# Performance work log

Measured on AMD Instinct MI355X. Metric: run time of the kernel, lower is better.

The kernel has to match this reference:

```python
import jax, jax.numpy as jnp
import numpy as np

N_NODES = 100000
N_EDGES = 1600000
NODE_DIM = 5
HIDDEN = 64
N_LAYERS = 3


def setup_inputs() -> dict:
    key = jax.random.key(0)
    ks = jax.random.split(key, 12)
    s = 0.1
    return {
        "x": jax.random.normal(ks[0], (N_NODES, NODE_DIM), dtype=jnp.float32),
        "edge_index": jax.random.randint(ks[1], (2, N_EDGES), 0, N_NODES, dtype=jnp.int32),
        # message MLP params per layer (stacked over layers)
        "W1": jax.random.normal(ks[2], (N_LAYERS, 2 * NODE_DIM, HIDDEN), dtype=jnp.float32) * s,
        "b1": jnp.zeros((N_LAYERS, HIDDEN), dtype=jnp.float32),
        "W2": jax.random.normal(ks[3], (N_LAYERS, HIDDEN, NODE_DIM), dtype=jnp.float32) * s,
        "b2": jnp.zeros((N_LAYERS, NODE_DIM), dtype=jnp.float32),
        # update MLP params per layer
        "U1": jax.random.normal(ks[4], (N_LAYERS, 2 * NODE_DIM, HIDDEN), dtype=jnp.float32) * s,
        "bu1": jnp.zeros((N_LAYERS, HIDDEN), dtype=jnp.float32),
        "U2": jax.random.normal(ks[5], (N_LAYERS, HIDDEN, NODE_DIM), dtype=jnp.float32) * s,
        "bu2": jnp.zeros((N_LAYERS, NODE_DIM), dtype=jnp.float32),
        # readout
        "Wr": jax.random.normal(ks[6], (NODE_DIM, NODE_DIM), dtype=jnp.float32) * s,
        "br": jnp.zeros((NODE_DIM,), dtype=jnp.float32),
    }


def reference(x, edge_index, W1, b1, W2, b2, U1, bu1, U2, bu2, Wr, br):
    # PyG convention: messages flow from source j = edge_index[0] to target i = edge_index[1]
    src = edge_index[0]
    dst = edge_index[1]
    n = x.shape[0]
    for l in range(N_LAYERS):
        x_i = x[dst]                                   # [E, d] target features
        x_j = x[src]                                   # [E, d] source features
        msg_in = jnp.concatenate([x_i, x_j], axis=-1)  # [E, 2d]
        msg = jax.nn.relu(msg_in @ W1[l] + b1[l]) @ W2[l] + b2[l]   # [E, d]
        aggr = jax.ops.segment_sum(msg, dst, num_segments=n)        # [N, d] scatter-add at targets
        upd_in = jnp.concatenate([x, aggr], axis=-1)   # [N, 2d]
        upd = jax.nn.relu(upd_in @ U1[l] + bu1[l]) @ U2[l] + bu2[l]  # [N, d]
        x = upd + x                                    # residual (in SkeletonGNN.forward)
    return x @ Wr + br
```

## Files before the change

kernel.cpp:

```cpp
#include <hip/hip_runtime.h>

#define N_NODES 100000
#define N_EDGES 1600000
#define DIM 5
#define HID 64
#define N_LAYERS 3
#define SCAN_BLK 256
#define NBLK ((N_NODES + SCAN_BLK - 1) / SCAN_BLK)

__global__ __launch_bounds__(256) void fused_hist_msg1_kernel(
    const float* __restrict__ x,
    const int* __restrict__ ei,
    const float* __restrict__ W1, const float* __restrict__ b1,
    const float* __restrict__ W2, const float* __restrict__ b2,
    int* __restrict__ cnt, int* __restrict__ rank,
    float* __restrict__ msg0)
{
    int e = blockIdx.x * blockDim.x + threadIdx.x;
    if (e >= N_EDGES) return;
    int src = ei[e];
    int dst = ei[N_EDGES + e];

    int rk = atomicAdd(&cnt[dst], 1);

    float in[10];
    const float* xi = x + (long)dst * DIM;
    const float* xj = x + (long)src * DIM;
#pragma unroll
    for (int d = 0; d < DIM; ++d) in[d] = xi[d];
#pragma unroll
    for (int d = 0; d < DIM; ++d) in[DIM + d] = xj[d];

    float msg[DIM];
#pragma unroll
    for (int j = 0; j < DIM; ++j) msg[j] = b2[j];

#pragma unroll 8
    for (int h = 0; h < HID; ++h) {
        float acc = b1[h];
#pragma unroll
        for (int d = 0; d < 10; ++d) acc = fmaf(in[d], W1[d * HID + h], acc);
        acc = fmaxf(acc, 0.0f);
#pragma unroll
        for (int j = 0; j < DIM; ++j) msg[j] = fmaf(acc, W2[h * DIM + j], msg[j]);
    }

    float* mp = msg0 + (long)e * DIM;
#pragma unroll
    for (int j = 0; j < DIM; ++j) mp[j] = msg[j];

    rank[e] = rk;
}


__global__ __launch_bounds__(SCAN_BLK) void scan_part_kernel(
    const int* __restrict__ cnt, int* __restrict__ blk_sum)
{
    __shared__ int s[SCAN_BLK];
    int t = threadIdx.x;
    int i = blockIdx.x * SCAN_BLK + t;
    s[t] = (i < N_NODES) ? cnt[i] : 0;
    __syncthreads();
    for (int off = SCAN_BLK / 2; off > 0; off >>= 1) {
        if (t < off) s[t] += s[t + off];
        __syncthreads();
    }
    if (t == 0) blk_sum[blockIdx.x] = s[0];
}

__global__ __launch_bounds__(512) void scan_blk_kernel(
    const int* __restrict__ blk_sum, int* __restrict__ blk_pref)
{
    __shared__ int s[512];
    int t = threadIdx.x;
    int v = (t < NBLK) ? blk_sum[t] : 0;
    s[t] = v;
    __syncthreads();
    for (int off = 1; off < 512; off <<= 1) {
        int a = (t >= off) ? s[t - off] : 0;
        __syncthreads();
        s[t] += a;
        __syncthreads();
    }
    if (t < NBLK) blk_pref[t] = s[t] - v;
}

__global__ __launch_bounds__(SCAN_BLK) void scan_add_kernel(
    const int* __restrict__ cnt, const int* __restrict__ blk_pref,
    int* __restrict__ row_ptr)
{
    __shared__ int s[SCAN_BLK];
    int t = threadIdx.x;
    int i = blockIdx.x * SCAN_BLK + t;
    int c = (i < N_NODES) ? cnt[i] : 0;
    s[t] = c;
    __syncthreads();
    for (int off = 1; off < SCAN_BLK; off <<= 1) {
        int a = (t >= off) ? s[t - off] : 0;
        __syncthreads();
        s[t] += a;
        __syncthreads();
    }
    if (i < N_NODES) row_ptr[i] = blk_pref[blockIdx.x] + s[t] - c;
    if (i == 0) row_ptr[N_NODES] = N_EDGES;
}

__global__ __launch_bounds__(256) void scatter_pair_perm_kernel(
    const int* __restrict__ ei, const int* __restrict__ rank,
    const int* __restrict__ row_ptr,
    int2* __restrict__ spair, int* __restrict__ eperm)
{
    int e = blockIdx.x * blockDim.x + threadIdx.x;
    if (e >= N_EDGES) return;
    int src = ei[e];
    int dst = ei[N_EDGES + e];
    int pos = row_ptr[dst] + rank[e];
    spair[pos] = make_int2(src, dst);
    eperm[pos] = e;
}

__global__ __launch_bounds__(256) void edge_msg_reduce_kernel(
    const float* __restrict__ x,
    const int2* __restrict__ spair,
    const float* __restrict__ W1, const float* __restrict__ b1,
    const float* __restrict__ W2, const float* __restrict__ b2,
    float* __restrict__ aggr)
{
    __shared__ float lmsg[256][DIM];
    __shared__ int ldst[256];

    int tid = threadIdx.x;
    int e0 = blockIdx.x * 256;
    int bsize = N_EDGES - e0;
    if (bsize > 256) bsize = 256;
    bool active = tid < bsize;

    int src = 0, dst = -1;
    if (active) {
        int2 p = spair[e0 + tid];
        src = p.x; dst = p.y;
    }
    ldst[tid] = dst;

    float msg[DIM] = {0.f, 0.f, 0.f, 0.f, 0.f};
    if (active) {
        float in[10];
        const float* xi = x + (long)dst * DIM;
        const float* xj = x + (long)src * DIM;
#pragma unroll
        for (int d = 0; d < DIM; ++d) in[d] = xi[d];
#pragma unroll
        for (int d = 0; d < DIM; ++d) in[DIM + d] = xj[d];
#pragma unroll
        for (int j = 0; j < DIM; ++j) msg[j] = b2[j];
#pragma unroll 8
        for (int h = 0; h < HID; ++h) {
            float acc = b1[h];
#pragma unroll
            for (int d = 0; d < 10; ++d) acc = fmaf(in[d], W1[d * HID + h], acc);
            acc = fmaxf(acc, 0.0f);
#pragma unroll
            for (int j = 0; j < DIM; ++j) msg[j] = fmaf(acc, W2[h * DIM + j], msg[j]);
        }
    }
#pragma unroll
    for (int j = 0; j < DIM; ++j) lmsg[tid][j] = msg[j];
    __syncthreads();

    if (active && (tid == 0 || ldst[tid - 1] != dst)) {
        float acc[DIM];
#pragma unroll
        for (int j = 0; j < DIM; ++j) acc[j] = msg[j];
        int i = tid + 1;
        while (i < bsize && ldst[i] == dst) {
#pragma unroll
            for (int j = 0; j < DIM; ++j) acc[j] += lmsg[i][j];
            ++i;
        }
        float* ap = aggr + (long)dst * DIM;
        if (tid == 0 || i == bsize) {
#pragma unroll
            for (int j = 0; j < DIM; ++j) atomicAdd(ap + j, acc[j]);
        } else {
#pragma unroll
            for (int j = 0; j < DIM; ++j) ap[j] = acc[j];
        }
    }
}

template <bool FINAL>
__global__ __launch_bounds__(256) void node_upd8_kernel(
    const float* __restrict__ x,
    const float* __restrict__ aggr,
    const float* __restrict__ U1, const float* __restrict__ bu1,
    const float* __restrict__ U2, const float* __restrict__ bu2,
    const float* __restrict__ Wr, const float* __restrict__ br,
    float* __restrict__ xout)
{
    int gt = blockIdx.x * blockDim.x + threadIdx.x;
    int v = gt >> 3;
    int r = gt & 7;
    if (v >= N_NODES) return;

    float in2[10];
#pragma unroll
    for (int d = 0; d < DIM; ++d) in2[d] = x[(long)v * DIM + d];
#pragma unroll
    for (int d = 0; d < DIM; ++d) in2[DIM + d] = aggr[(long)v * DIM + d];

    float upd[DIM] = {0.f, 0.f, 0.f, 0.f, 0.f};
#pragma unroll
    for (int hh = 0; hh < 8; ++hh) {
        int h = r + hh * 8;
        float acc = bu1[h];
#pragma unroll
        for (int d = 0; d < 10; ++d) acc = fmaf(in2[d], U1[d * HID + h], acc);
        acc = fmaxf(acc, 0.0f);
#pragma unroll
        for (int j = 0; j < DIM; ++j) upd[j] = fmaf(acc, U2[h * DIM + j], upd[j]);
    }
#pragma unroll
    for (int m = 1; m < 8; m <<= 1) {
#pragma unroll
        for (int j = 0; j < DIM; ++j) upd[j] += __shfl_xor(upd[j], m, 64);
    }

    if (r == 0) {
        float xn[DIM];
#pragma unroll
        for (int j = 0; j < DIM; ++j) xn[j] = upd[j] + bu2[j] + in2[j];
        if (FINAL) {
#pragma unroll
            for (int j = 0; j < DIM; ++j) {
                float o = br[j];
#pragma unroll
                for (int d = 0; d < DIM; ++d) o = fmaf(xn[d], Wr[d * DIM + j], o);
                xout[(long)v * DIM + j] = o;
            }
        } else {
#pragma unroll
            for (int j = 0; j < DIM; ++j) xout[(long)v * DIM + j] = xn[j];
        }
    }
}

template <bool FINAL, bool INDIRECT>
__global__ __launch_bounds__(256) void gather_update8_kernel(
    const float* __restrict__ x,
    const float* __restrict__ msg_buf,
    const int* __restrict__ eperm,
    const int* __restrict__ row_ptr,
    const float* __restrict__ U1, const float* __restrict__ bu1,
    const float* __restrict__ U2, const float* __restrict__ bu2,
    const float* __restrict__ Wr, const float* __restrict__ br,
    float* __restrict__ xout)
{
    int gt = blockIdx.x * blockDim.x + threadIdx.x;
    int v = gt >> 3;
    int r = gt & 7;
    if (v >= N_NODES) return;

    int s = row_ptr[v], e1 = row_ptr[v + 1];

    float agg[DIM] = {0.f, 0.f, 0.f, 0.f, 0.f};
    for (int e = s + r; e < e1; e += 8) {
        long me = INDIRECT ? (long)eperm[e] : (long)e;
        const float* mp = msg_buf + me * DIM;
#pragma unroll
        for (int j = 0; j < DIM; ++j) agg[j] += mp[j];
    }
#pragma unroll
    for (int m = 1; m < 8; m <<= 1) {
#pragma unroll
        for (int j = 0; j < DIM; ++j) agg[j] += __shfl_xor(agg[j], m, 64);
    }

    float in2[10];
#pragma unroll
    for (int d = 0; d < DIM; ++d) in2[d] = x[(long)v * DIM + d];
#pragma unroll
    for (int d = 0; d < DIM; ++d) in2[DIM + d] = agg[d];

    float upd[DIM] = {0.f, 0.f, 0.f, 0.f, 0.f};
#pragma unroll
    for (int hh = 0; hh < 8; ++hh) {
        int h = r + hh * 8;
        float acc = bu1[h];
#pragma unroll
        for (int d = 0; d < 10; ++d) acc = fmaf(in2[d], U1[d * HID + h], acc);
        acc = fmaxf(acc, 0.0f);
#pragma unroll
        for (int j = 0; j < DIM; ++j) upd[j] = fmaf(acc, U2[h * DIM + j], upd[j]);
    }
#pragma unroll
    for (int m = 1; m < 8; m <<= 1) {
#pragma unroll
        for (int j = 0; j < DIM; ++j) upd[j] += __shfl_xor(upd[j], m, 64);
    }

    if (r == 0) {
        float xn[DIM];
#pragma unroll
        for (int j = 0; j < DIM; ++j) xn[j] = upd[j] + bu2[j] + in2[j];
        if (FINAL) {
#pragma unroll
            for (int j = 0; j < DIM; ++j) {
                float o = br[j];
#pragma unroll
                for (int d = 0; d < DIM; ++d) o = fmaf(xn[d], Wr[d * DIM + j], o);
                xout[(long)v * DIM + j] = o;
            }
        } else {
#pragma unroll
            for (int j = 0; j < DIM; ++j) xout[(long)v * DIM + j] = xn[j];
        }
    }
}


__global__ __launch_bounds__(256) void edge_msg_kernel(
    const float* __restrict__ x, const int* __restrict__ ei,
    const float* __restrict__ W1, const float* __restrict__ b1,
    const float* __restrict__ W2, const float* __restrict__ b2,
    float* __restrict__ aggr)
{
    int e = blockIdx.x * blockDim.x + threadIdx.x;
    if (e >= N_EDGES) return;
    int src = ei[e];
    int dst = ei[N_EDGES + e];
    float in[10];
    const float* xi = x + (long)dst * DIM;
    const float* xj = x + (long)src * DIM;
#pragma unroll
    for (int d = 0; d < DIM; ++d) in[d] = xi[d];
#pragma unroll
    for (int d = 0; d < DIM; ++d) in[DIM + d] = xj[d];
    float msg[DIM];
#pragma unroll
    for (int j = 0; j < DIM; ++j) msg[j] = b2[j];
#pragma unroll 8
    for (int h = 0; h < HID; ++h) {
        float acc = b1[h];
#pragma unroll
        for (int d = 0; d < 10; ++d) acc = fmaf(in[d], W1[d * HID + h], acc);
        acc = fmaxf(acc, 0.0f);
#pragma unroll
        for (int j = 0; j < DIM; ++j) msg[j] = fmaf(acc, W2[h * DIM + j], msg[j]);
    }
    float* ap = aggr + (long)dst * DIM;
#pragma unroll
    for (int j = 0; j < DIM; ++j) atomicAdd(ap + j, msg[j]);
}

template <bool FINAL>
__global__ __launch_bounds__(256) void node_upd_kernel(
    const float* __restrict__ x, const float* __restrict__ aggr,
    const float* __restrict__ U1, const float* __restrict__ bu1,
    const float* __restrict__ U2, const float* __restrict__ bu2,
    const float* __restrict__ Wr, const float* __restrict__ br,
    float* __restrict__ xout)
{
    int v = blockIdx.x * blockDim.x + threadIdx.x;
    if (v >= N_NODES) return;
    float in[10];
#pragma unroll
    for (int d = 0; d < DIM; ++d) in[d] = x[(long)v * DIM + d];
#pragma unroll
    for (int d = 0; d < DIM; ++d) in[DIM + d] = aggr[(long)v * DIM + d];
    float upd[DIM];
#pragma unroll
    for (int j = 0; j < DIM; ++j) upd[j] = bu2[j];
#pragma unroll 8
    for (int h = 0; h < HID; ++h) {
        float acc = bu1[h];
#pragma unroll
        for (int d = 0; d < 10; ++d) acc = fmaf(in[d], U1[d * HID + h], acc);
        acc = fmaxf(acc, 0.0f);
#pragma unroll
        for (int j = 0; j < DIM; ++j) upd[j] = fmaf(acc, U2[h * DIM + j], upd[j]);
    }
    float xn[DIM];
#pragma unroll
    for (int j = 0; j < DIM; ++j) xn[j] = upd[j] + in[j];
    if (FINAL) {
#pragma unroll
        for (int j = 0; j < DIM; ++j) {
            float o = br[j];
#pragma unroll
            for (int d = 0; d < DIM; ++d) o = fmaf(xn[d], Wr[d * DIM + j], o);
            xout[(long)v * DIM + j] = o;
        }
    } else {
#pragma unroll
        for (int j = 0; j < DIM; ++j) xout[(long)v * DIM + j] = xn[j];
    }
}


static inline size_t alignup(size_t x) { return (x + 255) & ~(size_t)255; }

extern "C" void kernel_launch(void* const* d_in, const int* in_sizes, int n_in,
                              void* d_out, int out_size, void* d_ws, size_t ws_size,
                              hipStream_t stream) {
    const float* x   = (const float*)d_in[0];
    const int*   ei  = (const int*)d_in[1];
    const float* W1  = (const float*)d_in[2];
    const float* b1  = (const float*)d_in[3];
    const float* W2  = (const float*)d_in[4];
    const float* b2  = (const float*)d_in[5];
    const float* U1  = (const float*)d_in[6];
    const float* bu1 = (const float*)d_in[7];
    const float* U2  = (const float*)d_in[8];
    const float* bu2 = (const float*)d_in[9];
    const float* Wr  = (const float*)d_in[10];
    const float* br  = (const float*)d_in[11];
    float* out = (float*)d_out;

    char* ws = (char*)d_ws;

    size_t o_cnt  = 0;
    size_t o_row  = alignup(o_cnt + (size_t)N_NODES * 4);
    size_t o_bsum = alignup(o_row + (size_t)(N_NODES + 1) * 4);
    size_t o_bpre = alignup(o_bsum + (size_t)NBLK * 4);
    size_t o_sp   = alignup(o_bpre + (size_t)NBLK * 4);
    size_t o_perm = alignup(o_sp + (size_t)N_EDGES * 8);
    size_t o_rank = alignup(o_perm + (size_t)N_EDGES * 4);
    size_t o_xA   = alignup(o_rank + (size_t)N_EDGES * 4);
    size_t o_xB   = alignup(o_xA + (size_t)N_NODES * DIM * 4);
    size_t o_msg  = alignup(o_xB + (size_t)N_NODES * DIM * 4);
    size_t needed = o_msg + (size_t)N_EDGES * DIM * 4;

    dim3 blk(256);
    dim3 eg((N_EDGES + 255) / 256);
    dim3 ng((N_NODES + 255) / 256);
    dim3 ng8((N_NODES * 8 + 255) / 256);

    if (ws_size < needed) {
        size_t nbytes = (size_t)N_NODES * DIM * sizeof(float);
        float* aggr = (float*)ws;
        float* xA   = (float*)(ws + nbytes);
        float* xB   = (float*)(ws + 2 * nbytes);
        const float* xcur = x;
        for (int l = 0; l < N_LAYERS; ++l) {
            hipMemsetAsync(aggr, 0, nbytes, stream);
            edge_msg_kernel<<<eg, blk, 0, stream>>>(
                xcur, ei, W1 + l * 10 * HID, b1 + l * HID,
                W2 + l * HID * DIM, b2 + l * DIM, aggr);
            if (l < N_LAYERS - 1) {
                float* xn = (l == 0) ? xA : xB;
                node_upd_kernel<false><<<ng, blk, 0, stream>>>(
                    xcur, aggr, U1 + l * 10 * HID, bu1 + l * HID,
                    U2 + l * HID * DIM, bu2 + l * DIM, Wr, br, xn);
                xcur = xn;
            } else {
                node_upd_kernel<true><<<ng, blk, 0, stream>>>(
                    xcur, aggr, U1 + l * 10 * HID, bu1 + l * HID,
                    U2 + l * HID * DIM, bu2 + l * DIM, Wr, br, out);
            }
        }
        return;
    }

    int* cnt      = (int*)(ws + o_cnt);
    int* row_ptr  = (int*)(ws + o_row);
    int* blk_sum  = (int*)(ws + o_bsum);
    int* blk_pref = (int*)(ws + o_bpre);
    int2* spair   = (int2*)(ws + o_sp);
    int* eperm    = (int*)(ws + o_perm);
    int* rank     = (int*)(ws + o_rank);
    float* xA     = (float*)(ws + o_xA);
    float* xB     = (float*)(ws + o_xB);
    float* msgbuf = (float*)(ws + o_msg);
    float* aggr   = (float*)(ws + o_msg);

    hipMemsetAsync(cnt, 0, (size_t)N_NODES * 4, stream);
    fused_hist_msg1_kernel<<<eg, blk, 0, stream>>>(
        x, ei, W1, b1, W2, b2, cnt, rank, msgbuf);

    scan_part_kernel<<<NBLK, SCAN_BLK, 0, stream>>>(cnt, blk_sum);
    scan_blk_kernel<<<1, 512, 0, stream>>>(blk_sum, blk_pref);
    scan_add_kernel<<<NBLK, SCAN_BLK, 0, stream>>>(cnt, blk_pref, row_ptr);
    scatter_pair_perm_kernel<<<eg, blk, 0, stream>>>(ei, rank, row_ptr, spair, eperm);

    gather_update8_kernel<false, true><<<ng8, blk, 0, stream>>>(
        x, msgbuf, eperm, row_ptr, U1, bu1, U2, bu2, Wr, br, xA);

    hipMemsetAsync(aggr, 0, (size_t)N_NODES * DIM * 4, stream);
    edge_msg_reduce_kernel<<<eg, blk, 0, stream>>>(
        xA, spair, W1 + 10 * HID, b1 + HID, W2 + HID * DIM, b2 + DIM, aggr);
    node_upd8_kernel<false><<<ng8, blk, 0, stream>>>(
        xA, aggr, U1 + 10 * HID, bu1 + HID,
        U2 + HID * DIM, bu2 + DIM, Wr, br, xB);

    hipMemsetAsync(aggr, 0, (size_t)N_NODES * DIM * 4, stream);
    edge_msg_reduce_kernel<<<eg, blk, 0, stream>>>(
        xB, spair, W1 + 2 * 10 * HID, b1 + 2 * HID,
        W2 + 2 * HID * DIM, b2 + 2 * DIM, aggr);
    node_upd8_kernel<true><<<ng8, blk, 0, stream>>>(
        xB, aggr, U1 + 2 * 10 * HID, bu1 + 2 * HID,
        U2 + 2 * HID * DIM, bu2 + 2 * DIM, Wr, br, out);
}
```

Before: 401.2 us.

## Fuse edge message MLP and aggregation into per-node CSR update kernel

Layers 2 and 3 now run one node-centric kernel per layer. Eight lanes per node walk that node's CSR incoming edges, compute the message MLP with the destination half of W1 precomputed once per node, reduce across lanes, and apply the update MLP directly. This removes the aggr memsets, the atomics, the separate edge kernel and the aggr round trip through memory, and it halves the sorted edge array to sources only. In exchange, work per node is serialized over its degree, which can cause load imbalance, and each edge is handled by 8 lanes that split the hidden units.

```diff
diff --git a/kernel.cpp b/kernel.cpp
--- a/kernel.cpp
+++ b/kernel.cpp
@@ -105,93 +105,27 @@
     if (i == 0) row_ptr[N_NODES] = N_EDGES;
 }
 
-__global__ __launch_bounds__(256) void scatter_pair_perm_kernel(
+__global__ __launch_bounds__(256) void scatter_src_perm_kernel(
     const int* __restrict__ ei, const int* __restrict__ rank,
     const int* __restrict__ row_ptr,
-    int2* __restrict__ spair, int* __restrict__ eperm)
+    int* __restrict__ ssrc, int* __restrict__ eperm)
 {
     int e = blockIdx.x * blockDim.x + threadIdx.x;
     if (e >= N_EDGES) return;
     int src = ei[e];
     int dst = ei[N_EDGES + e];
     int pos = row_ptr[dst] + rank[e];
-    spair[pos] = make_int2(src, dst);
+    ssrc[pos] = src;
     eperm[pos] = e;
 }
 
-__global__ __launch_bounds__(256) void edge_msg_reduce_kernel(
+template <bool FINAL>
+__global__ __launch_bounds__(256) void node_layer8_kernel(
     const float* __restrict__ x,
-    const int2* __restrict__ spair,
+    const int* __restrict__ ssrc,
+    const int* __restrict__ row_ptr,
     const float* __restrict__ W1, const float* __restrict__ b1,
     const float* __restrict__ W2, const float* __restrict__ b2,
-    float* __restrict__ aggr)
-{
-    __shared__ float lmsg[256][DIM];
-    __shared__ int ldst[256];
-
-    int tid = threadIdx.x;
-    int e0 = blockIdx.x * 256;
-    int bsize = N_EDGES - e0;
-    if (bsize > 256) bsize = 256;
-    bool active = tid < bsize;
-
-    int src = 0, dst = -1;
-    if (active) {
-        int2 p = spair[e0 + tid];
-        src = p.x; dst = p.y;
-    }
-    ldst[tid] = dst;
-
-    float msg[DIM] = {0.f, 0.f, 0.f, 0.f, 0.f};
-    if (active) {
-        float in[10];
-        const float* xi = x + (long)dst * DIM;
-        const float* xj = x + (long)src * DIM;
-#pragma unroll
-        for (int d = 0; d < DIM; ++d) in[d] = xi[d];
-#pragma unroll
-        for (int d = 0; d < DIM; ++d) in[DIM + d] = xj[d];
-#pragma unroll
-        for (int j = 0; j < DIM; ++j) msg[j] = b2[j];
-#pragma unroll 8
-        for (int h = 0; h < HID; ++h) {
-            float acc = b1[h];
-#pragma unroll
-            for (int d = 0; d < 10; ++d) acc = fmaf(in[d], W1[d * HID + h], acc);
-            acc = fmaxf(acc, 0.0f);
-#pragma unroll
-            for (int j = 0; j < DIM; ++j) msg[j] = fmaf(acc, W2[h * DIM + j], msg[j]);
-        }
-    }
-#pragma unroll
-    for (int j = 0; j < DIM; ++j) lmsg[tid][j] = msg[j];
-    __syncthreads();
-
-    if (active && (tid == 0 || ldst[tid - 1] != dst)) {
-        float acc[DIM];
-#pragma unroll
-        for (int j = 0; j < DIM; ++j) acc[j] = msg[j];
-        int i = tid + 1;
-        while (i < bsize && ldst[i] == dst) {
-#pragma unroll
-            for (int j = 0; j < DIM; ++j) acc[j] += lmsg[i][j];
-            ++i;
-        }
-        float* ap = aggr + (long)dst * DIM;
-        if (tid == 0 || i == bsize) {
-#pragma unroll
-            for (int j = 0; j < DIM; ++j) atomicAdd(ap + j, acc[j]);
-        } else {
-#pragma unroll
-            for (int j = 0; j < DIM; ++j) ap[j] = acc[j];
-        }
-    }
-}
-
-template <bool FINAL>
-__global__ __launch_bounds__(256) void node_upd8_kernel(
-    const float* __restrict__ x,
-    const float* __restrict__ aggr,
     const float* __restrict__ U1, const float* __restrict__ bu1,
     const float* __restrict__ U2, const float* __restrict__ bu2,
     const float* __restrict__ Wr, const float* __restrict__ br,
@@ -202,11 +136,55 @@
     int r = gt & 7;
     if (v >= N_NODES) return;
 
+    float xv[DIM];
+#pragma unroll
+    for (int d = 0; d < DIM; ++d) xv[d] = x[(long)v * DIM + d];
+
+    float hd[8];
+#pragma unroll
+    for (int hh = 0; hh < 8; ++hh) {
+        int h = r + hh * 8;
+        float a = b1[h];
+#pragma unroll
+        for (int d = 0; d < DIM; ++d) a = fmaf(xv[d], W1[d * HID + h], a);
+        hd[hh] = a;
+    }
+
+    int s = row_ptr[v], e1 = row_ptr[v + 1];
+    float agg[DIM] = {0.f, 0.f, 0.f, 0.f, 0.f};
+
+    for (int e = s; e < e1; ++e) {
+        int src = ssrc[e];
+        float xs[DIM];
+        const float* xp = x + (long)src * DIM;
+#pragma unroll
+        for (int d = 0; d < DIM; ++d) xs[d] = xp[d];
+
+#pragma unroll
+        for (int hh = 0; hh < 8; ++hh) {
+            int h = r + hh * 8;
+            float a = hd[hh];
+#pragma unroll
+            for (int d = 0; d < DIM; ++d) a = fmaf(xs[d], W1[(DIM + d) * HID + h], a);
+            a = fmaxf(a, 0.0f);
+#pragma unroll
+            for (int j = 0; j < DIM; ++j) agg[j] = fmaf(a, W2[h * DIM + j], agg[j]);
+        }
+    }
+#pragma unroll
+    for (int m = 1; m < 8; m <<= 1) {
+#pragma unroll
+        for (int j = 0; j < DIM; ++j) agg[j] += __shfl_xor(agg[j], m, 64);
+    }
+    float degf = (float)(e1 - s);
+#pragma unroll
+    for (int j = 0; j < DIM; ++j) agg[j] = fmaf(degf, b2[j], agg[j]);
+
     float in2[10];
 #pragma unroll
-    for (int d = 0; d < DIM; ++d) in2[d] = x[(long)v * DIM + d];
-#pragma unroll
-    for (int d = 0; d < DIM; ++d) in2[DIM + d] = aggr[(long)v * DIM + d];
+    for (int d = 0; d < DIM; ++d) in2[d] = xv[d];
+#pragma unroll
+    for (int d = 0; d < DIM; ++d) in2[DIM + d] = agg[d];
 
     float upd[DIM] = {0.f, 0.f, 0.f, 0.f, 0.f};
 #pragma unroll
@@ -228,7 +206,7 @@
     if (r == 0) {
         float xn[DIM];
 #pragma unroll
-        for (int j = 0; j < DIM; ++j) xn[j] = upd[j] + bu2[j] + in2[j];
+        for (int j = 0; j < DIM; ++j) xn[j] = upd[j] + bu2[j] + xv[j];
         if (FINAL) {
 #pragma unroll
             for (int j = 0; j < DIM; ++j) {
@@ -422,8 +400,8 @@
     size_t o_row  = alignup(o_cnt + (size_t)N_NODES * 4);
     size_t o_bsum = alignup(o_row + (size_t)(N_NODES + 1) * 4);
     size_t o_bpre = alignup(o_bsum + (size_t)NBLK * 4);
-    size_t o_sp   = alignup(o_bpre + (size_t)NBLK * 4);
-    size_t o_perm = alignup(o_sp + (size_t)N_EDGES * 8);
+    size_t o_ssrc = alignup(o_bpre + (size_t)NBLK * 4);
+    size_t o_perm = alignup(o_ssrc + (size_t)N_EDGES * 4);
     size_t o_rank = alignup(o_perm + (size_t)N_EDGES * 4);
     size_t o_xA   = alignup(o_rank + (size_t)N_EDGES * 4);
     size_t o_xB   = alignup(o_xA + (size_t)N_NODES * DIM * 4);
@@ -465,13 +443,12 @@
     int* row_ptr  = (int*)(ws + o_row);
     int* blk_sum  = (int*)(ws + o_bsum);
     int* blk_pref = (int*)(ws + o_bpre);
-    int2* spair   = (int2*)(ws + o_sp);
+    int* ssrc     = (int*)(ws + o_ssrc);
     int* eperm    = (int*)(ws + o_perm);
     int* rank     = (int*)(ws + o_rank);
     float* xA     = (float*)(ws + o_xA);
     float* xB     = (float*)(ws + o_xB);
     float* msgbuf = (float*)(ws + o_msg);
-    float* aggr   = (float*)(ws + o_msg);
 
     hipMemsetAsync(cnt, 0, (size_t)N_NODES * 4, stream);
     fused_hist_msg1_kernel<<<eg, blk, 0, stream>>>(
@@ -480,23 +457,19 @@
     scan_part_kernel<<<NBLK, SCAN_BLK, 0, stream>>>(cnt, blk_sum);
     scan_blk_kernel<<<1, 512, 0, stream>>>(blk_sum, blk_pref);
     scan_add_kernel<<<NBLK, SCAN_BLK, 0, stream>>>(cnt, blk_pref, row_ptr);
-    scatter_pair_perm_kernel<<<eg, blk, 0, stream>>>(ei, rank, row_ptr, spair, eperm);
+    scatter_src_perm_kernel<<<eg, blk, 0, stream>>>(ei, rank, row_ptr, ssrc, eperm);
 
     gather_update8_kernel<false, true><<<ng8, blk, 0, stream>>>(
         x, msgbuf, eperm, row_ptr, U1, bu1, U2, bu2, Wr, br, xA);
 
-    hipMemsetAsync(aggr, 0, (size_t)N_NODES * DIM * 4, stream);
-    edge_msg_reduce_kernel<<<eg, blk, 0, stream>>>(
-        xA, spair, W1 + 10 * HID, b1 + HID, W2 + HID * DIM, b2 + DIM, aggr);
-    node_upd8_kernel<false><<<ng8, blk, 0, stream>>>(
-        xA, aggr, U1 + 10 * HID, bu1 + HID,
-        U2 + HID * DIM, bu2 + DIM, Wr, br, xB);
-
-    hipMemsetAsync(aggr, 0, (size_t)N_NODES * DIM * 4, stream);
-    edge_msg_reduce_kernel<<<eg, blk, 0, stream>>>(
-        xB, spair, W1 + 2 * 10 * HID, b1 + 2 * HID,
-        W2 + 2 * HID * DIM, b2 + 2 * DIM, aggr);
-    node_upd8_kernel<true><<<ng8, blk, 0, stream>>>(
-        xB, aggr, U1 + 2 * 10 * HID, bu1 + 2 * HID,
-        U2 + 2 * HID * DIM, bu2 + 2 * DIM, Wr, br, out);
-}
+    node_layer8_kernel<false><<<ng8, blk, 0, stream>>>(
+        xA, ssrc, row_ptr, W1 + 10 * HID, b1 + HID,
+        W2 + HID * DIM, b2 + DIM,
+        U1 + 10 * HID, bu1 + HID, U2 + HID * DIM, bu2 + DIM, Wr, br, xB);
+
+    node_layer8_kernel<true><<<ng8, blk, 0, stream>>>(
+        xB, ssrc, row_ptr, W1 + 2 * 10 * HID, b1 + 2 * HID,
+        W2 + 2 * HID * DIM, b2 + 2 * DIM,
+        U1 + 2 * 10 * HID, bu1 + 2 * HID, U2 + 2 * HID * DIM, bu2 + 2 * DIM,
+        Wr, br, out);
+}
```

New measurement: 436.3 us. +8.8%, slower.
